# Performance work log

Hardware: AMD Instinct MI355X
Metric: run time of the kernel (lower is better)

Reference implementation:

```python
import jax, jax.numpy as jnp
import numpy as np


def setup_inputs() -> dict:
    key = jax.random.key(0)
    k_v, k_w = jax.random.split(key)
    L, N, H, D = 2048, 8, 16, 64
    v = jax.random.normal(k_v, (N, L, H, D), dtype=jnp.float32)
    # torch init: self.w.data.uniform_(-0.1, 0.1) overwrites the sorted randn
    w = jax.random.uniform(k_w, (L,), dtype=jnp.float32, minval=-0.1, maxval=0.1)
    return {"v": v, "w": w}


def _toeplitz_bias(w):
    # Faithful to _construnct_bias: p = [flip(w[1:]), w], bias[i, j] = p[L-1 - i + j]
    # which is the symmetric Toeplitz matrix bias[i, j] = w[|i - j|].
    L = w.shape[0]
    idx = jnp.abs(jnp.arange(L)[:, None] - jnp.arange(L)[None, :])  # [L, L]
    return w[idx]


def reference(v, w):
    # PositionalBias._naive
    L = w.shape[0]
    bias = _toeplitz_bias(w)                      # [L, L]
    z_pb = bias.sum(-1).reshape(1, L, 1)          # [1, L, 1]
    pbv = jnp.einsum('nlhd,lj->njhd', v, bias)    # [N, L, H, D]
    return pbv, z_pb
```

## Files before the change

### kernel.cpp

```cpp
#include <hip/hip_runtime.h>
#include <hip/hip_bf16.h>

#define L 2048
#define HD 1024
#define NB 8
#define NT 32
#define PROW 4096

using f32x4 = __attribute__((ext_vector_type(4))) float;
using fl4   = __attribute__((ext_vector_type(4))) float;
using s16x8 = __attribute__((ext_vector_type(8))) short;

__device__ __forceinline__ short f2bf(float f) {
    __hip_bfloat16 h = __float2bfloat16(f);
    short s;
    __builtin_memcpy(&s, &h, 2);
    return s;
}

__device__ __forceinline__ void gload_lds16(const void* g, void* l) {
    __builtin_amdgcn_global_load_lds(
        (const __attribute__((address_space(1))) unsigned int*)g,
        (__attribute__((address_space(3))) unsigned int*)l, 16, 0, 0);
}

__global__ __launch_bounds__(256) void pb_prep(const float* __restrict__ w,
                                               short* __restrict__ p8) {
    int idx = blockIdx.x * 256 + threadIdx.x;
    int s = idx >> 12;
    int x = idx & (PROW - 1);
    int k = x + s;
    short val = 0;
    if (k <= 4094) {
        int d = k - 2047; d = d < 0 ? -d : d;
        val = f2bf(w[d]);
    }
    p8[idx] = val;
}

__global__ __launch_bounds__(256) void pb_vtile(const float* __restrict__ v,
                                                s16x8* __restrict__ vt) {
    __shared__ __align__(16) short Ts[256 * 64];
    const int kk = blockIdx.x, cg4 = blockIdx.y, n = blockIdx.z;
    const int l0 = kk * 64, c0 = cg4 * 256;
    const int t = threadIdx.x;
    const float* vn = v + (size_t)n * L * HD;

    #pragma unroll
    for (int i = 0; i < 16; ++i) {
        int unit = i * 256 + t;
        int l = unit >> 6, cq = unit & 63;
        fl4 x = *(const fl4*)&vn[(size_t)(l0 + l) * HD + c0 + cq * 4];
        int lsub = l & 7, lblk = l >> 3;
        #pragma unroll
        for (int j = 0; j < 4; ++j) {
            int c = cq * 4 + j;
            Ts[c * 64 + ((lblk ^ ((c >> 2) & 7)) << 3) + lsub] = f2bf(x[j]);
        }
    }
    __syncthreads();

    s16x8* outp = vt + ((size_t)(n * NT + kk) * 1024 + c0) * 8;
    #pragma unroll
    for (int i2 = 0; i2 < 8; ++i2) {
        int ci = i2 * 256 + t;
        int c = ci >> 3, h = ci & 7;
        int slot = h ^ ((c >> 2) & 7);
        outp[ci] = *(const s16x8*)&Ts[c * 64 + slot * 8];
    }
}

__global__ __launch_bounds__(256, 2) void pb_gemm4(const short* __restrict__ p8,
                                                   const short* __restrict__ vt,
                                                   float* __restrict__ out) {
    __shared__ __align__(16) short lds_[32768];

    const int bid = blockIdx.x;
    const int cm = bid & 7;
    const int n  = (bid >> 3) & 7;
    const int jm = bid >> 6;
    const int j0 = jm * 128;
    const int c0 = cm * 128;

    const int t = threadIdx.x;
    const int lane = t & 63;
    const int w = t >> 6;
    const int wr = w >> 1, wc = w & 1;
    const int fr = lane & 15, fk = lane >> 4;

    int offA[4], offB[4];
    #pragma unroll
    for (int m = 0; m < 4; ++m) {
        int r = wr * 64 + m * 16 + fr;
        offA[m] = r * 128 + ((fk ^ (r & 7)) << 4);
    }
    #pragma unroll
    for (int nf = 0; nf < 4; ++nf) {
        int c = wc * 64 + nf * 16 + fr;
        offB[nf] = 16384 + c * 128 + ((fk ^ (c & 7)) << 4);
    }

    const short* srcA0; const short* srcA1; const short* srcA2; const short* srcA3;
    const short* srcB0; const short* srcB1; const short* srcB2; const short* srcB3;
    {
        const size_t bbase = ((size_t)(n * NT) * 1024 + c0) * 8ull;
        int dc, r, s, h, q, srow, c;
        dc = w * 256 + 0 * 64 + lane;
        r = dc >> 3; s = dc & 7; h = s ^ (r & 7);
        q = 2047 + h * 8 - j0 - r; srow = q & 7;
        srcA0 = p8 + srow * PROW + (q - srow);
        c = dc >> 3; h = (dc & 7) ^ (c & 7);
        srcB0 = (const short*)(vt + (bbase + (size_t)c * 8 + h) * 8);
        dc = w * 256 + 1 * 64 + lane;
        r = dc >> 3; s = dc & 7; h = s ^ (r & 7);
        q = 2047 + h * 8 - j0 - r; srow = q & 7;
        srcA1 = p8 + srow * PROW + (q - srow);
        c = dc >> 3; h = (dc & 7) ^ (c & 7);
        srcB1 = (const short*)(vt + (bbase + (size_t)c * 8 + h) * 8);
        dc = w * 256 + 2 * 64 + lane;
        r = dc >> 3; s = dc & 7; h = s ^ (r & 7);
        q = 2047 + h * 8 - j0 - r; srow = q & 7;
        srcA2 = p8 + srow * PROW + (q - srow);
        c = dc >> 3; h = (dc & 7) ^ (c & 7);
        srcB2 = (const short*)(vt + (bbase + (size_t)c * 8 + h) * 8);
        dc = w * 256 + 3 * 64 + lane;
        r = dc >> 3; s = dc & 7; h = s ^ (r & 7);
        q = 2047 + h * 8 - j0 - r; srow = q & 7;
        srcA3 = p8 + srow * PROW + (q - srow);
        c = dc >> 3; h = (dc & 7) ^ (c & 7);
        srcB3 = (const short*)(vt + (bbase + (size_t)c * 8 + h) * 8);
    }
    const int wA = w * 4096;

#define STAGE_ALL(base) { \
    gload_lds16(srcA0, (char*)lds_ + (base) + wA); \
    gload_lds16(srcA1, (char*)lds_ + (base) + wA + 1024); \
    gload_lds16(srcA2, (char*)lds_ + (base) + wA + 2048); \
    gload_lds16(srcA3, (char*)lds_ + (base) + wA + 3072); \
    gload_lds16(srcB0, (char*)lds_ + (base) + 16384 + wA); \
    gload_lds16(srcB1, (char*)lds_ + (base) + 16384 + wA + 1024); \
    gload_lds16(srcB2, (char*)lds_ + (base) + 16384 + wA + 2048); \
    gload_lds16(srcB3, (char*)lds_ + (base) + 16384 + wA + 3072); \
    srcA0 += 64; srcA1 += 64; srcA2 += 64; srcA3 += 64; \
    srcB0 += 65536; srcB1 += 65536; srcB2 += 65536; srcB3 += 65536; }

    STAGE_ALL(0);
    __syncthreads();

    f32x4 acc[4][4] = {};

    for (int T = 0; T < NT; ++T) {
        const char* bR = (const char*)lds_ + (T & 1) * 32768;

        if (T < NT - 1) {
            const int nb = ((T + 1) & 1) * 32768;
            STAGE_ALL(nb);
        }

        s16x8 af[4][2], bf[4][2];
        #pragma unroll
        for (int m = 0; m < 4; ++m) {
            af[m][0] = *(const s16x8*)(bR + offA[m]);
            af[m][1] = *(const s16x8*)(bR + (offA[m] ^ 64));
        }
        #pragma unroll
        for (int nf = 0; nf < 4; ++nf) {
            bf[nf][0] = *(const s16x8*)(bR + offB[nf]);
            bf[nf][1] = *(const s16x8*)(bR + (offB[nf] ^ 64));
        }

        __builtin_amdgcn_s_setprio(1);
        #pragma unroll
        for (int m = 0; m < 4; ++m)
            #pragma unroll
            for (int nf = 0; nf < 4; ++nf)
                #pragma unroll
                for (int ki = 0; ki < 2; ++ki)
                    acc[m][nf] = __builtin_amdgcn_mfma_f32_16x16x32_bf16(
                        af[m][ki], bf[nf][ki], acc[m][nf], 0, 0, 0);
        __builtin_amdgcn_s_setprio(0);

        __syncthreads();
    }

    float* outn = out + (size_t)n * L * HD;
    #pragma unroll
    for (int m = 0; m < 4; ++m) {
        const int row = j0 + wr * 64 + m * 16 + fk * 4;
        #pragma unroll
        for (int nf = 0; nf < 4; ++nf) {
            const int col = c0 + wc * 64 + nf * 16 + fr;
            #pragma unroll
            for (int r = 0; r < 4; ++r)
                outn[(size_t)(row + r) * HD + col] = acc[m][nf][r];
        }
    }
}

__global__ __launch_bounds__(256) void pb_z(const float* __restrict__ w,
                                            float* __restrict__ z) {
    __shared__ float part[256];
    __shared__ float S[L];
    const int t = threadIdx.x;
    float loc[8]; float s = 0.f;
    #pragma unroll
    for (int i = 0; i < 8; ++i) { loc[i] = w[t * 8 + i]; s += loc[i]; }
    part[t] = s;
    __syncthreads();
    if (t == 0) {
        float a = 0.f;
        for (int i = 0; i < 256; ++i) { float tmp = part[i]; part[i] = a; a += tmp; }
    }
    __syncthreads();
    float a = part[t];
    #pragma unroll
    for (int i = 0; i < 8; ++i) { a += loc[i]; S[t * 8 + i] = a; }
    __syncthreads();
    const float w0 = S[0];
    #pragma unroll
    for (int i = 0; i < 8; ++i) {
        int j = t * 8 + i;
        z[j] = S[j] + S[2047 - j] - w0;
    }
}

extern "C" void kernel_launch(void* const* d_in, const int* in_sizes, int n_in,
                              void* d_out, int out_size, void* d_ws, size_t ws_size,
                              hipStream_t stream) {
    const float* v = (const float*)d_in[0];
    const float* w = (const float*)d_in[1];
    float* out = (float*)d_out;

    short* p8 = (short*)d_ws;
    s16x8* vt = (s16x8*)((char*)d_ws + 65536);

    pb_prep<<<128, 256, 0, stream>>>(w, p8);
    pb_vtile<<<dim3(NT, 4, NB), 256, 0, stream>>>(v, vt);
    pb_gemm4<<<1024, 256, 0, stream>>>(p8, (const short*)vt, out);
    pb_z<<<1, 256, 0, stream>>>(w, out + (size_t)NB * L * HD);
}
```

Before: 84.51 us.

## Load GEMM fragments directly from global memory and merge z kernel into prep

The GEMM kernel drops its LDS double-buffering and barriers. Each wave now loads its MFMA A and B fragments straight from global memory, using a reorganised vtile layout that makes the B fragment loads coalesced per lane. The z prefix-sum computation is folded into an extra block of the prep kernel, which removes one kernel launch. The risk is higher global and L2 traffic, since wave fragments are no longer shared through LDS, and fragment load latency is exposed in a loop that is only unrolled by two.

```diff
diff --git a/kernel.cpp b/kernel.cpp
--- a/kernel.cpp
+++ b/kernel.cpp
@@ -18,24 +18,45 @@
     return s;
 }
 
-__device__ __forceinline__ void gload_lds16(const void* g, void* l) {
-    __builtin_amdgcn_global_load_lds(
-        (const __attribute__((address_space(1))) unsigned int*)g,
-        (__attribute__((address_space(3))) unsigned int*)l, 16, 0, 0);
-}
-
 __global__ __launch_bounds__(256) void pb_prep(const float* __restrict__ w,
-                                               short* __restrict__ p8) {
-    int idx = blockIdx.x * 256 + threadIdx.x;
-    int s = idx >> 12;
-    int x = idx & (PROW - 1);
-    int k = x + s;
-    short val = 0;
-    if (k <= 4094) {
-        int d = k - 2047; d = d < 0 ? -d : d;
-        val = f2bf(w[d]);
+                                               short* __restrict__ p8,
+                                               float* __restrict__ z) {
+    __shared__ float part[256];
+    __shared__ float S[L];
+    const int t = threadIdx.x;
+    if (blockIdx.x < 128) {
+        int idx = blockIdx.x * 256 + t;
+        int s = idx >> 12;
+        int x = idx & (PROW - 1);
+        int k = x + s;
+        short val = 0;
+        if (k <= 4094) {
+            int d = k - 2047; d = d < 0 ? -d : d;
+            val = f2bf(w[d]);
+        }
+        p8[idx] = val;
+    } else {
+        float loc[8]; float s = 0.f;
+        #pragma unroll
+        for (int i = 0; i < 8; ++i) { loc[i] = w[t * 8 + i]; s += loc[i]; }
+        part[t] = s;
+        __syncthreads();
+        if (t == 0) {
+            float a = 0.f;
+            for (int i = 0; i < 256; ++i) { float tmp = part[i]; part[i] = a; a += tmp; }
+        }
+        __syncthreads();
+        float a = part[t];
+        #pragma unroll
+        for (int i = 0; i < 8; ++i) { a += loc[i]; S[t * 8 + i] = a; }
+        __syncthreads();
+        const float w0 = S[0];
+        #pragma unroll
+        for (int i = 0; i < 8; ++i) {
+            int j = t * 8 + i;
+            z[j] = S[j] + S[2047 - j] - w0;
+        }
     }
-    p8[idx] = val;
 }
 
 __global__ __launch_bounds__(256) void pb_vtile(const float* __restrict__ v,
@@ -60,21 +81,20 @@
     }
     __syncthreads();
 
-    s16x8* outp = vt + ((size_t)(n * NT + kk) * 1024 + c0) * 8;
+    s16x8* outp = vt + ((size_t)(n * NT + kk) * 64 + cg4 * 16) * 128;
     #pragma unroll
     for (int i2 = 0; i2 < 8; ++i2) {
         int ci = i2 * 256 + t;
-        int c = ci >> 3, h = ci & 7;
+        int Gl = ci >> 7, h = (ci >> 4) & 7, cl = ci & 15;
+        int c = Gl * 16 + cl;
         int slot = h ^ ((c >> 2) & 7);
         outp[ci] = *(const s16x8*)&Ts[c * 64 + slot * 8];
     }
 }
 
-__global__ __launch_bounds__(256, 2) void pb_gemm4(const short* __restrict__ p8,
-                                                   const short* __restrict__ vt,
+__global__ __launch_bounds__(256, 2) void pb_gemmr(const short* __restrict__ p8,
+                                                   const s16x8* __restrict__ vt,
                                                    float* __restrict__ out) {
-    __shared__ __align__(16) short lds_[32768];
-
     const int bid = blockIdx.x;
     const int cm = bid & 7;
     const int n  = (bid >> 3) & 7;
@@ -88,86 +108,34 @@
     const int wr = w >> 1, wc = w & 1;
     const int fr = lane & 15, fk = lane >> 4;
 
-    int offA[4], offB[4];
+    int aoff[4][2];
     #pragma unroll
-    for (int m = 0; m < 4; ++m) {
-        int r = wr * 64 + m * 16 + fr;
-        offA[m] = r * 128 + ((fk ^ (r & 7)) << 4);
-    }
-    #pragma unroll
-    for (int nf = 0; nf < 4; ++nf) {
-        int c = wc * 64 + nf * 16 + fr;
-        offB[nf] = 16384 + c * 128 + ((fk ^ (c & 7)) << 4);
-    }
+    for (int m = 0; m < 4; ++m)
+        #pragma unroll
+        for (int ki = 0; ki < 2; ++ki) {
+            int r = wr * 64 + m * 16 + fr;
+            int idx0 = 2047 + ki * 32 + fk * 8 - j0 - r;
+            int srow = idx0 & 7;
+            aoff[m][ki] = srow * PROW + (idx0 - srow);
+        }
 
-    const short* srcA0; const short* srcA1; const short* srcA2; const short* srcA3;
-    const short* srcB0; const short* srcB1; const short* srcB2; const short* srcB3;
-    {
-        const size_t bbase = ((size_t)(n * NT) * 1024 + c0) * 8ull;
-        int dc, r, s, h, q, srow, c;
-        dc = w * 256 + 0 * 64 + lane;
-        r = dc >> 3; s = dc & 7; h = s ^ (r & 7);
-        q = 2047 + h * 8 - j0 - r; srow = q & 7;
-        srcA0 = p8 + srow * PROW + (q - srow);
-        c = dc >> 3; h = (dc & 7) ^ (c & 7);
-        srcB0 = (const short*)(vt + (bbase + (size_t)c * 8 + h) * 8);
-        dc = w * 256 + 1 * 64 + lane;
-        r = dc >> 3; s = dc & 7; h = s ^ (r & 7);
-        q = 2047 + h * 8 - j0 - r; srow = q & 7;
-        srcA1 = p8 + srow * PROW + (q - srow);
-        c = dc >> 3; h = (dc & 7) ^ (c & 7);
-        srcB1 = (const short*)(vt + (bbase + (size_t)c * 8 + h) * 8);
-        dc = w * 256 + 2 * 64 + lane;
-        r = dc >> 3; s = dc & 7; h = s ^ (r & 7);
-        q = 2047 + h * 8 - j0 - r; srow = q & 7;
-        srcA2 = p8 + srow * PROW + (q - srow);
-        c = dc >> 3; h = (dc & 7) ^ (c & 7);
-        srcB2 = (const short*)(vt + (bbase + (size_t)c * 8 + h) * 8);
-        dc = w * 256 + 3 * 64 + lane;
-        r = dc >> 3; s = dc & 7; h = s ^ (r & 7);
-        q = 2047 + h * 8 - j0 - r; srow = q & 7;
-        srcA3 = p8 + srow * PROW + (q - srow);
-        c = dc >> 3; h = (dc & 7) ^ (c & 7);
-        srcB3 = (const short*)(vt + (bbase + (size_t)c * 8 + h) * 8);
-    }
-    const int wA = w * 4096;
-
-#define STAGE_ALL(base) { \
-    gload_lds16(srcA0, (char*)lds_ + (base) + wA); \
-    gload_lds16(srcA1, (char*)lds_ + (base) + wA + 1024); \
-    gload_lds16(srcA2, (char*)lds_ + (base) + wA + 2048); \
-    gload_lds16(srcA3, (char*)lds_ + (base) + wA + 3072); \
-    gload_lds16(srcB0, (char*)lds_ + (base) + 16384 + wA); \
-    gload_lds16(srcB1, (char*)lds_ + (base) + 16384 + wA + 1024); \
-    gload_lds16(srcB2, (char*)lds_ + (base) + 16384 + wA + 2048); \
-    gload_lds16(srcB3, (char*)lds_ + (base) + 16384 + wA + 3072); \
-    srcA0 += 64; srcA1 += 64; srcA2 += 64; srcA3 += 64; \
-    srcB0 += 65536; srcB1 += 65536; srcB2 += 65536; srcB3 += 65536; }
-
-    STAGE_ALL(0);
-    __syncthreads();
+    const int bB = (n * NT * 64 + cm * 8 + wc * 4) * 128 + lane;
 
     f32x4 acc[4][4] = {};
 
+    #pragma unroll 2
     for (int T = 0; T < NT; ++T) {
-        const char* bR = (const char*)lds_ + (T & 1) * 32768;
-
-        if (T < NT - 1) {
-            const int nb = ((T + 1) & 1) * 32768;
-            STAGE_ALL(nb);
-        }
-
         s16x8 af[4][2], bf[4][2];
         #pragma unroll
-        for (int m = 0; m < 4; ++m) {
-            af[m][0] = *(const s16x8*)(bR + offA[m]);
-            af[m][1] = *(const s16x8*)(bR + (offA[m] ^ 64));
-        }
+        for (int m = 0; m < 4; ++m)
+            #pragma unroll
+            for (int ki = 0; ki < 2; ++ki)
+                af[m][ki] = *(const s16x8*)(p8 + (aoff[m][ki] + T * 64));
         #pragma unroll
-        for (int nf = 0; nf < 4; ++nf) {
-            bf[nf][0] = *(const s16x8*)(bR + offB[nf]);
-            bf[nf][1] = *(const s16x8*)(bR + (offB[nf] ^ 64));
-        }
+        for (int nf = 0; nf < 4; ++nf)
+            #pragma unroll
+            for (int ki = 0; ki < 2; ++ki)
+                bf[nf][ki] = vt[bB + T * 8192 + nf * 128 + ki * 64];
 
         __builtin_amdgcn_s_setprio(1);
         #pragma unroll
@@ -179,8 +147,6 @@
                     acc[m][nf] = __builtin_amdgcn_mfma_f32_16x16x32_bf16(
                         af[m][ki], bf[nf][ki], acc[m][nf], 0, 0, 0);
         __builtin_amdgcn_s_setprio(0);
-
-        __syncthreads();
     }
 
     float* outn = out + (size_t)n * L * HD;
@@ -197,33 +163,6 @@
     }
 }
 
-__global__ __launch_bounds__(256) void pb_z(const float* __restrict__ w,
-                                            float* __restrict__ z) {
-    __shared__ float part[256];
-    __shared__ float S[L];
-    const int t = threadIdx.x;
-    float loc[8]; float s = 0.f;
-    #pragma unroll
-    for (int i = 0; i < 8; ++i) { loc[i] = w[t * 8 + i]; s += loc[i]; }
-    part[t] = s;
-    __syncthreads();
-    if (t == 0) {
-        float a = 0.f;
-        for (int i = 0; i < 256; ++i) { float tmp = part[i]; part[i] = a; a += tmp; }
-    }
-    __syncthreads();
-    float a = part[t];
-    #pragma unroll
-    for (int i = 0; i < 8; ++i) { a += loc[i]; S[t * 8 + i] = a; }
-    __syncthreads();
-    const float w0 = S[0];
-    #pragma unroll
-    for (int i = 0; i < 8; ++i) {
-        int j = t * 8 + i;
-        z[j] = S[j] + S[2047 - j] - w0;
-    }
-}
-
 extern "C" void kernel_launch(void* const* d_in, const int* in_sizes, int n_in,
                               void* d_out, int out_size, void* d_ws, size_t ws_size,
                               hipStream_t stream) {
@@ -234,8 +173,7 @@
     short* p8 = (short*)d_ws;
     s16x8* vt = (s16x8*)((char*)d_ws + 65536);
 
-    pb_prep<<<128, 256, 0, stream>>>(w, p8);
+    pb_prep<<<129, 256, 0, stream>>>(w, p8, out + (size_t)NB * L * HD);
     pb_vtile<<<dim3(NT, 4, NB), 256, 0, stream>>>(v, vt);
-    pb_gemm4<<<1024, 256, 0, stream>>>(p8, (const short*)vt, out);
-    pb_z<<<1, 256, 0, stream>>>(w, out + (size_t)NB * L * HD);
+    pb_gemmr<<<1024, 256, 0, stream>>>(p8, vt, out);
 }
```

New measurement: 156.9 us. +85.7%, slower.

## Deepen GEMM pipeline with register double-buffering and fold z into prep kernel

Applied to the files above, without the earlier changes.

The bf16 MFMA main loop now keeps two LDS tiles in flight. It double-buffers the A/B fragments in registers, so LDS reads for the next tile overlap the MFMAs of the current tile. Explicit vmcnt/lgkmcnt waits and raw s_barrier replace __syncthreads. The separate single-block z prefix-sum kernel becomes an extra block of the prep kernel, saving one launch. The cost is more register pressure from the doubled fragment arrays, which may hurt occupancy at the two-blocks-per-CU launch bound, plus hand-managed wait counts that are fragile.

```diff
diff --git a/kernel.cpp b/kernel.cpp
--- a/kernel.cpp
+++ b/kernel.cpp
@@ -25,17 +25,44 @@
 }
 
 __global__ __launch_bounds__(256) void pb_prep(const float* __restrict__ w,
-                                               short* __restrict__ p8) {
-    int idx = blockIdx.x * 256 + threadIdx.x;
-    int s = idx >> 12;
-    int x = idx & (PROW - 1);
-    int k = x + s;
-    short val = 0;
-    if (k <= 4094) {
-        int d = k - 2047; d = d < 0 ? -d : d;
-        val = f2bf(w[d]);
-    }
-    p8[idx] = val;
+                                               short* __restrict__ p8,
+                                               float* __restrict__ z) {
+    __shared__ float part[256];
+    __shared__ float S[L];
+    const int t = threadIdx.x;
+    if (blockIdx.x < 128) {
+        int idx = blockIdx.x * 256 + t;
+        int s = idx >> 12;
+        int x = idx & (PROW - 1);
+        int k = x + s;
+        short val = 0;
+        if (k <= 4094) {
+            int d = k - 2047; d = d < 0 ? -d : d;
+            val = f2bf(w[d]);
+        }
+        p8[idx] = val;
+    } else {
+        float loc[8]; float s = 0.f;
+        #pragma unroll
+        for (int i = 0; i < 8; ++i) { loc[i] = w[t * 8 + i]; s += loc[i]; }
+        part[t] = s;
+        __syncthreads();
+        if (t == 0) {
+            float a = 0.f;
+            for (int i = 0; i < 256; ++i) { float tmp = part[i]; part[i] = a; a += tmp; }
+        }
+        __syncthreads();
+        float a = part[t];
+        #pragma unroll
+        for (int i = 0; i < 8; ++i) { a += loc[i]; S[t * 8 + i] = a; }
+        __syncthreads();
+        const float w0 = S[0];
+        #pragma unroll
+        for (int i = 0; i < 8; ++i) {
+            int j = t * 8 + i;
+            z[j] = S[j] + S[2047 - j] - w0;
+        }
+    }
 }
 
 __global__ __launch_bounds__(256) void pb_vtile(const float* __restrict__ v,
@@ -144,44 +171,66 @@
     srcA0 += 64; srcA1 += 64; srcA2 += 64; srcA3 += 64; \
     srcB0 += 65536; srcB1 += 65536; srcB2 += 65536; srcB3 += 65536; }
 
+#define VMC8()  { asm volatile("s_waitcnt vmcnt(8)" ::: "memory"); \
+                  __builtin_amdgcn_sched_barrier(0); }
+#define VMC0()  { asm volatile("s_waitcnt vmcnt(0)" ::: "memory"); \
+                  __builtin_amdgcn_sched_barrier(0); }
+#define LGKM0() { asm volatile("s_waitcnt lgkmcnt(0)" ::: "memory"); \
+                  __builtin_amdgcn_sched_barrier(0); }
+#define BARR()  __builtin_amdgcn_s_barrier()
+
+#define READ_FRAGS(AF, BF, base) { \
+    const char* _b = (const char*)lds_ + (base); \
+    _Pragma("unroll") \
+    for (int m = 0; m < 4; ++m) { \
+        AF[m][0] = *(const s16x8*)(_b + offA[m]); \
+        AF[m][1] = *(const s16x8*)(_b + (offA[m] ^ 64)); \
+    } \
+    _Pragma("unroll") \
+    for (int nf = 0; nf < 4; ++nf) { \
+        BF[nf][0] = *(const s16x8*)(_b + offB[nf]); \
+        BF[nf][1] = *(const s16x8*)(_b + (offB[nf] ^ 64)); \
+    } \
+    __builtin_amdgcn_sched_barrier(0); }
+
+#define MFMA_ALL(AF, BF) { \
+    __builtin_amdgcn_s_setprio(1); \
+    _Pragma("unroll") \
+    for (int m = 0; m < 4; ++m) \
+        _Pragma("unroll") \
+        for (int nf = 0; nf < 4; ++nf) \
+            _Pragma("unroll") \
+            for (int ki = 0; ki < 2; ++ki) \
+                acc[m][nf] = __builtin_amdgcn_mfma_f32_16x16x32_bf16( \
+                    AF[m][ki], BF[nf][ki], acc[m][nf], 0, 0, 0); \
+    __builtin_amdgcn_s_setprio(0); }
+
+#define BODY(P, CURA, CURB, NXTA, NXTB, DO_STAGE, VMCN) { \
+    if (DO_STAGE) STAGE_ALL((P) * 32768); \
+    VMCN(); \
+    BARR(); \
+    READ_FRAGS(NXTA, NXTB, ((P) ^ 1) * 32768); \
+    MFMA_ALL(CURA, CURB); \
+    LGKM0(); \
+    BARR(); }
+
+    f32x4 acc[4][4] = {};
+    s16x8 afX[4][2], bfX[4][2], afY[4][2], bfY[4][2];
+
     STAGE_ALL(0);
-    __syncthreads();
-
-    f32x4 acc[4][4] = {};
-
-    for (int T = 0; T < NT; ++T) {
-        const char* bR = (const char*)lds_ + (T & 1) * 32768;
-
-        if (T < NT - 1) {
-            const int nb = ((T + 1) & 1) * 32768;
-            STAGE_ALL(nb);
-        }
-
-        s16x8 af[4][2], bf[4][2];
-        #pragma unroll
-        for (int m = 0; m < 4; ++m) {
-            af[m][0] = *(const s16x8*)(bR + offA[m]);
-            af[m][1] = *(const s16x8*)(bR + (offA[m] ^ 64));
-        }
-        #pragma unroll
-        for (int nf = 0; nf < 4; ++nf) {
-            bf[nf][0] = *(const s16x8*)(bR + offB[nf]);
-            bf[nf][1] = *(const s16x8*)(bR + (offB[nf] ^ 64));
-        }
-
-        __builtin_amdgcn_s_setprio(1);
-        #pragma unroll
-        for (int m = 0; m < 4; ++m)
-            #pragma unroll
-            for (int nf = 0; nf < 4; ++nf)
-                #pragma unroll
-                for (int ki = 0; ki < 2; ++ki)
-                    acc[m][nf] = __builtin_amdgcn_mfma_f32_16x16x32_bf16(
-                        af[m][ki], bf[nf][ki], acc[m][nf], 0, 0, 0);
-        __builtin_amdgcn_s_setprio(0);
-
-        __syncthreads();
-    }
+    STAGE_ALL(32768);
+    VMC8();
+    BARR();
+    READ_FRAGS(afX, bfX, 0);
+    LGKM0();
+    BARR();
+
+    for (int T = 0; T < NT - 2; T += 2) {
+        BODY(0, afX, bfX, afY, bfY, true, VMC8);
+        BODY(1, afY, bfY, afX, bfX, true, VMC8);
+    }
+    BODY(0, afX, bfX, afY, bfY, false, VMC0);
+    MFMA_ALL(afY, bfY);
 
     float* outn = out + (size_t)n * L * HD;
     #pragma unroll
@@ -194,33 +243,6 @@
             for (int r = 0; r < 4; ++r)
                 outn[(size_t)(row + r) * HD + col] = acc[m][nf][r];
         }
-    }
-}
-
-__global__ __launch_bounds__(256) void pb_z(const float* __restrict__ w,
-                                            float* __restrict__ z) {
-    __shared__ float part[256];
-    __shared__ float S[L];
-    const int t = threadIdx.x;
-    float loc[8]; float s = 0.f;
-    #pragma unroll
-    for (int i = 0; i < 8; ++i) { loc[i] = w[t * 8 + i]; s += loc[i]; }
-    part[t] = s;
-    __syncthreads();
-    if (t == 0) {
-        float a = 0.f;
-        for (int i = 0; i < 256; ++i) { float tmp = part[i]; part[i] = a; a += tmp; }
-    }
-    __syncthreads();
-    float a = part[t];
-    #pragma unroll
-    for (int i = 0; i < 8; ++i) { a += loc[i]; S[t * 8 + i] = a; }
-    __syncthreads();
-    const float w0 = S[0];
-    #pragma unroll
-    for (int i = 0; i < 8; ++i) {
-        int j = t * 8 + i;
-        z[j] = S[j] + S[2047 - j] - w0;
     }
 }
 
@@ -234,8 +256,7 @@
     short* p8 = (short*)d_ws;
     s16x8* vt = (s16x8*)((char*)d_ws + 65536);
 
-    pb_prep<<<128, 256, 0, stream>>>(w, p8);
+    pb_prep<<<129, 256, 0, stream>>>(w, p8, out + (size_t)NB * L * HD);
     pb_vtile<<<dim3(NT, 4, NB), 256, 0, stream>>>(v, vt);
     pb_gemm4<<<1024, 256, 0, stream>>>(p8, (const short*)vt, out);
-    pb_z<<<1, 256, 0, stream>>>(w, out + (size_t)NB * L * HD);
-}
+}
```

Result: faster. 81.91 us (-3.1%).
